# Optimization experiments

Hardware: AMD Instinct MI355X
Metric: run time of the kernel (lower is better)

## Reference

```python
import jax, jax.numpy as jnp
import numpy as np

DIM = 768
NUM_BLOCKS = 4
BLOCK = DIM // NUM_BLOCKS
SCALE = 0.02
LAMBDA = 0.01
EPS = 1e-5


def setup_inputs() -> dict:
    key = jax.random.key(0)
    ks = jax.random.split(key, 6)
    B, H, W = 64, 32, 32
    x = jax.random.normal(ks[0], (B, DIM, H, W), dtype=jnp.float32)
    w1 = jax.random.normal(ks[1], (2, NUM_BLOCKS, BLOCK, BLOCK), dtype=jnp.float32) * SCALE
    w2 = jax.random.normal(ks[2], (2, NUM_BLOCKS, BLOCK, BLOCK), dtype=jnp.float32) * SCALE
    b1 = jax.random.normal(ks[3], (2, NUM_BLOCKS, BLOCK), dtype=jnp.float32) * SCALE
    b2 = jax.random.normal(ks[4], (2, NUM_BLOCKS, BLOCK), dtype=jnp.float32) * SCALE
    gamma = jnp.ones((DIM,), dtype=jnp.float32)
    beta = jnp.zeros((DIM,), dtype=jnp.float32)
    return {"x": x, "w1": w1, "w2": w2, "b1": b1, "b2": b2,
            "gamma": gamma, "beta": beta, "H": H, "W": W}


def _softshrink(s, lam):
    return jnp.where(s > lam, s - lam, jnp.where(s < -lam, s + lam, jnp.zeros_like(s)))


def reference(x, w1, w2, b1, b2, gamma, beta, H, W):
    B, C = x.shape[0], x.shape[1]
    nb, bs = NUM_BLOCKS, C // NUM_BLOCKS
    # (B, C, H, W) -> (B, N, C)
    xt = x.reshape(B, C, H * W).transpose(0, 2, 1)
    residual = xt
    # LayerNorm over channel dim
    mu = jnp.mean(xt, axis=-1, keepdims=True)
    var = jnp.mean(jnp.square(xt - mu), axis=-1, keepdims=True)
    xn = (xt - mu) / jnp.sqrt(var + EPS) * gamma + beta
    # (B, N, nb, bs), FFT2 over (N, nb)
    xf = jnp.fft.fft2(xn.reshape(B, H * W, nb, bs), axes=(1, 2), norm='ortho')
    xr, xi = xf.real, xf.imag

    def mul(u, w):
        return jnp.einsum('bnqd,qdk->bnqk', u, w)  # block-diagonal matmul

    r1 = jax.nn.relu(mul(xr, w1[0]) - mul(xi, w1[1]) + b1[0])
    i1 = jax.nn.relu(mul(xr, w1[1]) + mul(xi, w1[0]) + b1[1])
    r2 = mul(r1, w2[0]) - mul(i1, w2[1]) + b2[0]
    i2 = mul(r1, w2[1]) + mul(i1, w2[0]) + b2[1]
    s = jnp.stack([r2, i2], axis=-1)
    s = _softshrink(s, LAMBDA)
    xc = jax.lax.complex(s[..., 0], s[..., 1])
    y = jnp.fft.ifft2(xc, axes=(1, 2), norm='ortho').real  # cast complex->real keeps real part
    y = y.reshape(B, H * W, C) + residual
    return y.transpose(0, 2, 1).reshape(B, C, H, W)
```

## Files before the change

kernel.cpp:

```cpp
#include <hip/hip_runtime.h>
#include <math.h>

#define BB 64
#define CC 768
#define NN 1024
#define BS 192
#define EPS 1e-5f
#define LAM 0.01f

typedef float  f32x4  __attribute__((ext_vector_type(4)));
typedef short  bf16x8 __attribute__((ext_vector_type(8)));

__device__ inline unsigned f2bf(float x) {
    unsigned u = __float_as_uint(x);
    u += 0x7fff + ((u >> 16) & 1);
    return u >> 16;
}
__device__ inline unsigned pack2(float r, float i) { return f2bf(r) | (f2bf(i) << 16); }
__device__ inline float bflo(unsigned v) { return __uint_as_float(v << 16); }
__device__ inline float bfhi(unsigned v) { return __uint_as_float(v & 0xffff0000u); }

__device__ inline int swz(int i) { return i ^ (((i >> 4) & 3) << 2); }

__global__ __launch_bounds__(512) void ln_stats(const float* __restrict__ x,
                                                float* __restrict__ mu,
                                                float* __restrict__ rstd) {
    int tn = threadIdx.x & 63, tc = threadIdx.x >> 6;
    int n = blockIdx.x * 256 + tn * 4, b = blockIdx.y;
    const float* xp = x + (size_t)b * CC * NN + n;
    f32x4 s = (f32x4)0.f, ss = (f32x4)0.f;
    #pragma unroll 4
    for (int c = tc; c < CC; c += 8) {
        f32x4 v = *(const f32x4*)(xp + (size_t)c * NN);
        s += v; ss += v * v;
    }
    __shared__ f32x4 sm[8][64], sq[8][64];
    sm[tc][tn] = s; sq[tc][tn] = ss;
    __syncthreads();
    if (tc == 0) {
        f32x4 S  = sm[0][tn], SS = sq[0][tn];
        #pragma unroll
        for (int i = 1; i < 8; i++) { S += sm[i][tn]; SS += sq[i][tn]; }
        f32x4 m = S * (1.f / 768.f);
        f32x4 r;
        #pragma unroll
        for (int i = 0; i < 4; i++) {
            float var = SS[i] * (1.f / 768.f) - m[i] * m[i];
            r[i] = rsqrtf(var + EPS);
        }
        *(f32x4*)(mu + (size_t)b * NN + n)   = m;
        *(f32x4*)(rstd + (size_t)b * NN + n) = r;
    }
}

__global__ void fwd_fft(const float* __restrict__ x,
                        const float* __restrict__ mu_, const float* __restrict__ rs_,
                        const float* __restrict__ gamma, const float* __restrict__ beta,
                        unsigned* __restrict__ Xp) {
    __shared__ float2 bufs[4][1024];
    int d = blockIdx.x, b = blockIdx.y, tid = threadIdx.x;

    const float* mp = mu_ + b * NN;
    const float* rp = rs_ + b * NN;
    #pragma unroll
    for (int q = 0; q < 4; q++) {
        int c = q * BS + d;
        float g = gamma[c], be = beta[c];
        const float* xp = x + ((size_t)b * CC + c) * NN;
        #pragma unroll
        for (int k = 0; k < 4; k++) {
            int n = tid + 256 * k;
            float v = (xp[n] - mp[n]) * rp[n] * g + be;
            bufs[q][swz(n)] = make_float2(v, 0.f);
        }
    }
    __syncthreads();

    #pragma unroll
    for (int sL = 0; sL < 4; sL++) {
        const int L = 256 >> (2 * sL);
        int j = tid & (L - 1);
        int base = ((tid - j) << 2) + j;
        float s1, c1;
        __sincosf(-(float)M_PI * 0.5f * (float)j / (float)L, &s1, &c1);
        float c2 = c1 * c1 - s1 * s1, s2 = 2.f * c1 * s1;
        float c3 = c2 * c1 - s2 * s1, s3 = c2 * s1 + s2 * c1;
        #pragma unroll
        for (int q = 0; q < 4; q++) {
            float2 a  = bufs[q][swz(base)];
            float2 bb = bufs[q][swz(base + L)];
            float2 cc = bufs[q][swz(base + 2 * L)];
            float2 dd = bufs[q][swz(base + 3 * L)];
            float t0r = a.x + cc.x, t0i = a.y + cc.y;
            float t1r = a.x - cc.x, t1i = a.y - cc.y;
            float t2r = bb.x + dd.x, t2i = bb.y + dd.y;
            float t3r = bb.x - dd.x, t3i = bb.y - dd.y;
            float X0r = t0r + t2r, X0i = t0i + t2i;
            float X2r = t0r - t2r, X2i = t0i - t2i;
            float X1r = t1r + t3i, X1i = t1i - t3r;
            float X3r = t1r - t3i, X3i = t1i + t3r;
            bufs[q][swz(base)]         = make_float2(X0r, X0i);
            bufs[q][swz(base + L)]     = make_float2(X1r * c1 - X1i * s1, X1r * s1 + X1i * c1);
            bufs[q][swz(base + 2 * L)] = make_float2(X2r * c2 - X2i * s2, X2r * s2 + X2i * c2);
            bufs[q][swz(base + 3 * L)] = make_float2(X3r * c3 - X3i * s3, X3r * s3 + X3i * c3);
        }
        __syncthreads();
    }

    float Xr[4][4], Xi[4][4];
    int i0 = swz(4 * tid);
    #pragma unroll
    for (int q = 0; q < 4; q++) {
        const float4* p = (const float4*)&bufs[q][i0];
        float4 u0 = p[0], u1 = p[1];
        float t0r = u0.x + u1.x, t0i = u0.y + u1.y;
        float t1r = u0.x - u1.x, t1i = u0.y - u1.y;
        float t2r = u0.z + u1.z, t2i = u0.w + u1.w;
        float t3r = u0.z - u1.z, t3i = u0.w - u1.w;
        Xr[q][0] = t0r + t2r; Xi[q][0] = t0i + t2i;
        Xr[q][1] = t1r + t3i; Xi[q][1] = t1i - t3r;
        Xr[q][2] = t0r - t2r; Xi[q][2] = t0i - t2i;
        Xr[q][3] = t1r - t3i; Xi[q][3] = t1i + t3r;
    }
    const float sc = 1.f / 64.f;
    unsigned o0[4], o1[4], o2[4], o3[4];
    #pragma unroll
    for (int m = 0; m < 4; m++) {
        float x0r = Xr[0][m], x0i = Xi[0][m];
        float x1r = Xr[1][m], x1i = Xi[1][m];
        float x2r = Xr[2][m], x2i = Xi[2][m];
        float x3r = Xr[3][m], x3i = Xi[3][m];
        float X0r = x0r + x1r + x2r + x3r, X0i = x0i + x1i + x2i + x3i;
        float X2r = x0r - x1r + x2r - x3r, X2i = x0i - x1i + x2i - x3i;
        float X1r = x0r + x1i - x2r - x3i, X1i = x0i - x1r - x2i + x3r;
        float X3r = x0r - x1i - x2r + x3i, X3i = x0i + x1r - x2i - x3r;
        o0[m] = pack2(X0r * sc, X0i * sc);
        o1[m] = pack2(X1r * sc, X1i * sc);
        o2[m] = pack2(X2r * sc, X2i * sc);
        o3[m] = pack2(X3r * sc, X3i * sc);
    }
    size_t qs = (size_t)BS * NN;
    int cs = ((d >> 2) & 3) << 3;
    size_t base = (((size_t)b * 4) * BS + d) * NN + ((4 * tid) ^ cs);
    *(uint4*)(Xp + base)          = make_uint4(o0[0], o0[1], o0[2], o0[3]);
    *(uint4*)(Xp + base + qs)     = make_uint4(o1[0], o1[1], o1[2], o1[3]);
    *(uint4*)(Xp + base + 2 * qs) = make_uint4(o2[0], o2[1], o2[2], o2[3]);
    *(uint4*)(Xp + base + 3 * qs) = make_uint4(o3[0], o3[1], o3[2], o3[3]);
}

__global__ void pack_b(const float* __restrict__ w, unsigned* __restrict__ Bp) {
    int ch = blockIdx.x, nblk = blockIdx.y, q = blockIdx.z;
    size_t tile = (size_t)((q * 3 + nblk) * 12 + ch);
    const float* wr = w + (size_t)q * BS * BS;
    const float* wi = w + (size_t)(4 + q) * BS * BS;
    for (int r = 0; r < 8; r++) {
        int idx = r * 256 + threadIdx.x;
        int jl = idx & 127, dd = idx >> 7;
        int j = nblk * 128 + jl;
        int h = j >> 1;
        int dg = ch * 16 + dd;
        float Wr = wr[(size_t)dg * BS + h];
        float Wi = wi[(size_t)dg * BS + h];
        unsigned v = (j & 1) ? pack2(Wi, Wr) : pack2(Wr, -Wi);
        int col = ((dd >> 2) ^ ((jl >> 1) & 3)) * 4 + (dd & 3);
        Bp[tile * 2048 + jl * 16 + col] = v;
    }
}

template <int ACT>
__global__ __launch_bounds__(256) void gemm_mlp(const unsigned* __restrict__ Ap,
                                                const unsigned* __restrict__ Bp,
                                                const float* __restrict__ bias,
                                                unsigned* __restrict__ Cp) {
    __shared__ unsigned sa[2][2048];
    __shared__ unsigned sb[2][2048];

    const int mblk = blockIdx.x;
    const int nblk = blockIdx.y;
    const int bq   = blockIdx.z;
    const int q    = bq & 3;
    const int tid  = threadIdx.x;
    const int wave = tid >> 6;
    const int lane = tid & 63;
    const int l15  = lane & 15;
    const int quad = lane >> 4;
    const int wm   = (wave & 1) * 64;
    const int wn   = (wave >> 1) * 64;

    const unsigned* a_base = Ap + ((size_t)bq * BS) * NN + mblk * 128;
    const size_t a_lane = (size_t)(lane >> 5) * NN + (lane & 31) * 4;
    const unsigned* b_tiles = Bp + (size_t)((q * 3 + nblk) * 12) * 2048;
    const int fgrp = (quad ^ ((l15 >> 1) & 3)) * 16;
    const int r0 = wave * 4;

    f32x4 acc[4][4];
    #pragma unroll
    for (int i = 0; i < 4; i++)
        #pragma unroll
        for (int j = 0; j < 4; j++)
            acc[i][j] = (f32x4)0.f;

    auto STAGE = [&](int ch, int buf) {
        const unsigned* ga = a_base + (size_t)(ch * 16) * NN;
        __builtin_amdgcn_global_load_lds(
            (const __attribute__((address_space(1))) unsigned*)(ga + (size_t)r0 * NN + a_lane),
            (__attribute__((address_space(3))) unsigned*)(&sa[buf][r0 * 128]), 16, 0, 0);
        __builtin_amdgcn_global_load_lds(
            (const __attribute__((address_space(1))) unsigned*)(ga + (size_t)(r0 + 2) * NN + a_lane),
            (__attribute__((address_space(3))) unsigned*)(&sa[buf][(r0 + 2) * 128]), 16, 0, 0);
        const unsigned* gb = b_tiles + (size_t)ch * 2048 + wave * 512;
        __builtin_amdgcn_global_load_lds(
            (const __attribute__((address_space(1))) unsigned*)(gb + lane * 4),
            (__attribute__((address_space(3))) unsigned*)(&sb[buf][wave * 512]), 16, 0, 0);
        __builtin_amdgcn_global_load_lds(
            (const __attribute__((address_space(1))) unsigned*)(gb + 256 + lane * 4),
            (__attribute__((address_space(3))) unsigned*)(&sb[buf][wave * 512 + 256]), 16, 0, 0);
    };

    STAGE(0, 0);

    #pragma unroll
    for (int ch = 0; ch < 12; ch++) {
        const int buf = ch & 1;
        __syncthreads();
        if (ch < 11) STAGE(ch + 1, buf ^ 1);

        bf16x8 af[4], bfr[4];
        const unsigned* sap = sa[buf];
        #pragma unroll
        for (int t = 0; t < 4; t++) {
            int cx = (wm + t * 16 + l15) ^ (quad << 3);
            union { unsigned u[4]; bf16x8 v; } au;
            #pragma unroll
            for (int g = 0; g < 4; g++)
                au.u[g] = sap[(quad * 4 + g) * 128 + cx];
            af[t] = au.v;
            bfr[t] = *(const bf16x8*)((const char*)sb[buf] + (wn + t * 16 + l15) * 64 + fgrp);
        }
        #pragma unroll
        for (int tn = 0; tn < 4; tn++)
            #pragma unroll
            for (int tm = 0; tm < 4; tm++)
                acc[tn][tm] = __builtin_amdgcn_mfma_f32_16x16x32_bf16(bfr[tn], af[tm], acc[tn][tm], 0, 0, 0);
    }

    #pragma unroll
    for (int tn = 0; tn < 4; tn++) {
        int jb = wn + tn * 16 + quad * 4;
        int hg = nblk * 64 + (jb >> 1);
        float b0r = bias[q * BS + hg];
        float b0i = bias[768 + q * BS + hg];
        float b1r = bias[q * BS + hg + 1];
        float b1i = bias[768 + q * BS + hg + 1];
        int s0 = ((hg >> 2) & 3) << 3;
        int s1 = (((hg + 1) >> 2) & 3) << 3;
        size_t row0 = ((size_t)bq * BS + hg) * NN + mblk * 128;
        #pragma unroll
        for (int tm = 0; tm < 4; tm++) {
            int mcol = wm + tm * 16 + l15;
            f32x4 a = acc[tn][tm];
            float v0 = a[0] + b0r, v1 = a[1] + b0i;
            float v2 = a[2] + b1r, v3 = a[3] + b1i;
            if (ACT == 0) {
                v0 = fmaxf(v0, 0.f); v1 = fmaxf(v1, 0.f);
                v2 = fmaxf(v2, 0.f); v3 = fmaxf(v3, 0.f);
            } else {
                v0 = (v0 > LAM) ? (v0 - LAM) : ((v0 < -LAM) ? (v0 + LAM) : 0.f);
                v1 = (v1 > LAM) ? (v1 - LAM) : ((v1 < -LAM) ? (v1 + LAM) : 0.f);
                v2 = (v2 > LAM) ? (v2 - LAM) : ((v2 < -LAM) ? (v2 + LAM) : 0.f);
                v3 = (v3 > LAM) ? (v3 - LAM) : ((v3 < -LAM) ? (v3 + LAM) : 0.f);
            }
            Cp[row0 + (mcol ^ s0)]      = pack2(v0, v1);
            Cp[row0 + NN + (mcol ^ s1)] = pack2(v2, v3);
        }
    }
}

__global__ void inv_fft(const float* __restrict__ x,
                        const unsigned* __restrict__ Yp,
                        float* __restrict__ out) {
    __shared__ float2 bufs[4][1024];
    int d = blockIdx.x, b = blockIdx.y, tid = threadIdx.x;

    float Ar[4][4], Ai[4][4];
    size_t qs = (size_t)BS * NN;
    int cs = ((d >> 2) & 3) << 3;
    size_t rowb = (((size_t)b * 4) * BS + d) * NN + ((4 * tid) ^ cs);
    #pragma unroll
    for (int q = 0; q < 4; q++) {
        uint4 v = *(const uint4*)(Yp + rowb + (size_t)q * qs);
        Ar[q][0] = bflo(v.x); Ai[q][0] = bfhi(v.x);
        Ar[q][1] = bflo(v.y); Ai[q][1] = bfhi(v.y);
        Ar[q][2] = bflo(v.z); Ai[q][2] = bfhi(v.z);
        Ar[q][3] = bflo(v.w); Ai[q][3] = bfhi(v.w);
    }
    #pragma unroll
    for (int m = 0; m < 4; m++) {
        float x0r = Ar[0][m], x0i = Ai[0][m];
        float x1r = Ar[1][m], x1i = Ai[1][m];
        float x2r = Ar[2][m], x2i = Ai[2][m];
        float x3r = Ar[3][m], x3i = Ai[3][m];
        float Y0r = x0r + x1r + x2r + x3r, Y0i = x0i + x1i + x2i + x3i;
        float Y2r = x0r - x1r + x2r - x3r, Y2i = x0i - x1i + x2i - x3i;
        float Y1r = x0r - x1i - x2r + x3i, Y1i = x0i + x1r - x2i - x3r;
        float Y3r = x0r + x1i - x2r - x3i, Y3i = x0i - x1r - x2i + x3r;
        Ar[0][m] = Y0r; Ai[0][m] = Y0i;
        Ar[1][m] = Y1r; Ai[1][m] = Y1i;
        Ar[2][m] = Y2r; Ai[2][m] = Y2i;
        Ar[3][m] = Y3r; Ai[3][m] = Y3i;
    }
    int i0 = swz(4 * tid);
    #pragma unroll
    for (int q = 0; q < 4; q++) {
        float t0r = Ar[q][0] + Ar[q][2], t0i = Ai[q][0] + Ai[q][2];
        float t1r = Ar[q][0] - Ar[q][2], t1i = Ai[q][0] - Ai[q][2];
        float t2r = Ar[q][1] + Ar[q][3], t2i = Ai[q][1] + Ai[q][3];
        float t3r = Ar[q][1] - Ar[q][3], t3i = Ai[q][1] - Ai[q][3];
        float4* p = (float4*)&bufs[q][i0];
        p[0] = make_float4(t0r + t2r, t0i + t2i, t1r - t3i, t1i + t3r);
        p[1] = make_float4(t0r - t2r, t0i - t2i, t1r + t3i, t1i - t3r);
    }
    __syncthreads();

    #pragma unroll
    for (int sL = 0; sL < 4; sL++) {
        const int L = 4 << (2 * sL);
        int j = tid & (L - 1);
        int base = ((tid - j) << 2) + j;
        float s1, c1;
        __sincosf((float)M_PI * 0.5f * (float)j / (float)L, &s1, &c1);
        float c2 = c1 * c1 - s1 * s1, s2 = 2.f * c1 * s1;
        float c3 = c2 * c1 - s2 * s1, s3 = c2 * s1 + s2 * c1;
        #pragma unroll
        for (int q = 0; q < 4; q++) {
            float2 y0 = bufs[q][swz(base)];
            float2 y1 = bufs[q][swz(base + L)];
            float2 y2 = bufs[q][swz(base + 2 * L)];
            float2 y3 = bufs[q][swz(base + 3 * L)];
            float A1r = y1.x * c1 - y1.y * s1, A1i = y1.x * s1 + y1.y * c1;
            float A2r = y2.x * c2 - y2.y * s2, A2i = y2.x * s2 + y2.y * c2;
            float A3r = y3.x * c3 - y3.y * s3, A3i = y3.x * s3 + y3.y * c3;
            float t0r = y0.x + A2r, t0i = y0.y + A2i;
            float t1r = y0.x - A2r, t1i = y0.y - A2i;
            float t2r = A1r + A3r, t2i = A1i + A3i;
            float t3r = A1r - A3r, t3i = A1i - A3i;
            bufs[q][swz(base)]         = make_float2(t0r + t2r, t0i + t2i);
            bufs[q][swz(base + L)]     = make_float2(t1r - t3i, t1i + t3r);
            bufs[q][swz(base + 2 * L)] = make_float2(t0r - t2r, t0i - t2i);
            bufs[q][swz(base + 3 * L)] = make_float2(t1r + t3i, t1i - t3r);
        }
        __syncthreads();
    }

    const float sc = 1.f / 64.f;
    #pragma unroll
    for (int q = 0; q < 4; q++) {
        size_t row = (((size_t)b * 4 + q) * BS + d) * NN;
        const float* xp = x + row;
        #pragma unroll
        for (int k = 0; k < 4; k++) {
            int n = tid + 256 * k;
            out[row + n] = bufs[q][swz(n)].x * sc + xp[n];
        }
    }
}

extern "C" void kernel_launch(void* const* d_in, const int* in_sizes, int n_in,
                              void* d_out, int out_size, void* d_ws, size_t ws_size,
                              hipStream_t stream) {
    const float* x     = (const float*)d_in[0];
    const float* w1    = (const float*)d_in[1];
    const float* w2    = (const float*)d_in[2];
    const float* b1    = (const float*)d_in[3];
    const float* b2    = (const float*)d_in[4];
    const float* gamma = (const float*)d_in[5];
    const float* beta  = (const float*)d_in[6];

    unsigned* Xp = (unsigned*)d_ws;
    float* mu    = (float*)d_ws + (size_t)BB * CC * NN;
    float* rstd  = mu + (size_t)BB * NN;
    unsigned* Bp1 = (unsigned*)(rstd + (size_t)BB * NN);
    unsigned* Bp2 = Bp1 + (size_t)4 * 3 * 12 * 2048;
    unsigned* Hp = (unsigned*)d_out;
    unsigned* Yp = Xp;

    pack_b<<<dim3(12, 3, 4), 256, 0, stream>>>(w1, Bp1);
    pack_b<<<dim3(12, 3, 4), 256, 0, stream>>>(w2, Bp2);
    ln_stats<<<dim3(NN / 256, BB), 512, 0, stream>>>(x, mu, rstd);
    fwd_fft<<<dim3(BS, BB), 256, 0, stream>>>(x, mu, rstd, gamma, beta, Xp);
    gemm_mlp<0><<<dim3(8, 3, 256), 256, 0, stream>>>(Xp, Bp1, b1, Hp);
    gemm_mlp<1><<<dim3(8, 3, 256), 256, 0, stream>>>(Hp, Bp2, b2, Yp);
    inv_fft<<<dim3(BS, BB), 256, 0, stream>>>(x, Yp, (float*)d_out);
}
```

Before: 798.6 us.

## Drop LDS staging in GEMM and load MFMA fragments directly from global

Removes the double-buffered LDS staging, the barriers and the XOR swizzles from the block-diagonal GEMM. Each lane now reads its A and B fragments straight from global memory, and the producer/consumer layouts (forward FFT pack, weight pack, epilogue store, inverse FFT read) are unswizzled to match. The aim is to cut barrier and LDS overhead, at the cost of losing shared reuse across waves. A fragments become scattered 4-byte loads with strided rows, and there is no prefetch overlap.

```diff
diff --git a/kernel.cpp b/kernel.cpp
--- a/kernel.cpp
+++ b/kernel.cpp
@@ -140,8 +140,7 @@
         o3[m] = pack2(X3r * sc, X3i * sc);
     }
     size_t qs = (size_t)BS * NN;
-    int cs = ((d >> 2) & 3) << 3;
-    size_t base = (((size_t)b * 4) * BS + d) * NN + ((4 * tid) ^ cs);
+    size_t base = (((size_t)b * 4) * BS + d) * NN + 4 * tid;
     *(uint4*)(Xp + base)          = make_uint4(o0[0], o0[1], o0[2], o0[3]);
     *(uint4*)(Xp + base + qs)     = make_uint4(o1[0], o1[1], o1[2], o1[3]);
     *(uint4*)(Xp + base + 2 * qs) = make_uint4(o2[0], o2[1], o2[2], o2[3]);
@@ -162,8 +161,7 @@
         float Wr = wr[(size_t)dg * BS + h];
         float Wi = wi[(size_t)dg * BS + h];
         unsigned v = (j & 1) ? pack2(Wi, Wr) : pack2(Wr, -Wi);
-        int col = ((dd >> 2) ^ ((jl >> 1) & 3)) * 4 + (dd & 3);
-        Bp[tile * 2048 + jl * 16 + col] = v;
+        Bp[tile * 2048 + jl * 16 + dd] = v;
     }
 }
 
@@ -172,9 +170,6 @@
                                                 const unsigned* __restrict__ Bp,
                                                 const float* __restrict__ bias,
                                                 unsigned* __restrict__ Cp) {
-    __shared__ unsigned sa[2][2048];
-    __shared__ unsigned sb[2][2048];
-
     const int mblk = blockIdx.x;
     const int nblk = blockIdx.y;
     const int bq   = blockIdx.z;
@@ -187,11 +182,8 @@
     const int wm   = (wave & 1) * 64;
     const int wn   = (wave >> 1) * 64;
 
-    const unsigned* a_base = Ap + ((size_t)bq * BS) * NN + mblk * 128;
-    const size_t a_lane = (size_t)(lane >> 5) * NN + (lane & 31) * 4;
-    const unsigned* b_tiles = Bp + (size_t)((q * 3 + nblk) * 12) * 2048;
-    const int fgrp = (quad ^ ((l15 >> 1) & 3)) * 16;
-    const int r0 = wave * 4;
+    const unsigned* a_lane = Ap + ((size_t)bq * BS + quad * 4) * NN + mblk * 128 + wm + l15;
+    const unsigned* b_lane = Bp + (size_t)((q * 3 + nblk) * 12) * 2048 + (wn + l15) * 16 + quad * 4;
 
     f32x4 acc[4][4];
     #pragma unroll
@@ -200,42 +192,21 @@
         for (int j = 0; j < 4; j++)
             acc[i][j] = (f32x4)0.f;
 
-    auto STAGE = [&](int ch, int buf) {
-        const unsigned* ga = a_base + (size_t)(ch * 16) * NN;
-        __builtin_amdgcn_global_load_lds(
-            (const __attribute__((address_space(1))) unsigned*)(ga + (size_t)r0 * NN + a_lane),
-            (__attribute__((address_space(3))) unsigned*)(&sa[buf][r0 * 128]), 16, 0, 0);
-        __builtin_amdgcn_global_load_lds(
-            (const __attribute__((address_space(1))) unsigned*)(ga + (size_t)(r0 + 2) * NN + a_lane),
-            (__attribute__((address_space(3))) unsigned*)(&sa[buf][(r0 + 2) * 128]), 16, 0, 0);
-        const unsigned* gb = b_tiles + (size_t)ch * 2048 + wave * 512;
-        __builtin_amdgcn_global_load_lds(
-            (const __attribute__((address_space(1))) unsigned*)(gb + lane * 4),
-            (__attribute__((address_space(3))) unsigned*)(&sb[buf][wave * 512]), 16, 0, 0);
-        __builtin_amdgcn_global_load_lds(
-            (const __attribute__((address_space(1))) unsigned*)(gb + 256 + lane * 4),
-            (__attribute__((address_space(3))) unsigned*)(&sb[buf][wave * 512 + 256]), 16, 0, 0);
-    };
-
-    STAGE(0, 0);
-
     #pragma unroll
     for (int ch = 0; ch < 12; ch++) {
-        const int buf = ch & 1;
-        __syncthreads();
-        if (ch < 11) STAGE(ch + 1, buf ^ 1);
-
+        const unsigned* ap = a_lane + (size_t)(ch * 16) * NN;
+        const unsigned* bp = b_lane + ch * 2048;
         bf16x8 af[4], bfr[4];
-        const unsigned* sap = sa[buf];
         #pragma unroll
         for (int t = 0; t < 4; t++) {
-            int cx = (wm + t * 16 + l15) ^ (quad << 3);
             union { unsigned u[4]; bf16x8 v; } au;
             #pragma unroll
             for (int g = 0; g < 4; g++)
-                au.u[g] = sap[(quad * 4 + g) * 128 + cx];
+                au.u[g] = ap[(size_t)g * NN + t * 16];
             af[t] = au.v;
-            bfr[t] = *(const bf16x8*)((const char*)sb[buf] + (wn + t * 16 + l15) * 64 + fgrp);
+            union { uint4 u4; bf16x8 v; } bu;
+            bu.u4 = *(const uint4*)(bp + t * 256);
+            bfr[t] = bu.v;
         }
         #pragma unroll
         for (int tn = 0; tn < 4; tn++)
@@ -252,8 +223,6 @@
         float b0i = bias[768 + q * BS + hg];
         float b1r = bias[q * BS + hg + 1];
         float b1i = bias[768 + q * BS + hg + 1];
-        int s0 = ((hg >> 2) & 3) << 3;
-        int s1 = (((hg + 1) >> 2) & 3) << 3;
         size_t row0 = ((size_t)bq * BS + hg) * NN + mblk * 128;
         #pragma unroll
         for (int tm = 0; tm < 4; tm++) {
@@ -270,8 +239,8 @@
                 v2 = (v2 > LAM) ? (v2 - LAM) : ((v2 < -LAM) ? (v2 + LAM) : 0.f);
                 v3 = (v3 > LAM) ? (v3 - LAM) : ((v3 < -LAM) ? (v3 + LAM) : 0.f);
             }
-            Cp[row0 + (mcol ^ s0)]      = pack2(v0, v1);
-            Cp[row0 + NN + (mcol ^ s1)] = pack2(v2, v3);
+            Cp[row0 + mcol]      = pack2(v0, v1);
+            Cp[row0 + NN + mcol] = pack2(v2, v3);
         }
     }
 }
@@ -284,8 +253,7 @@
 
     float Ar[4][4], Ai[4][4];
     size_t qs = (size_t)BS * NN;
-    int cs = ((d >> 2) & 3) << 3;
-    size_t rowb = (((size_t)b * 4) * BS + d) * NN + ((4 * tid) ^ cs);
+    size_t rowb = (((size_t)b * 4) * BS + d) * NN + 4 * tid;
     #pragma unroll
     for (int q = 0; q < 4; q++) {
         uint4 v = *(const uint4*)(Yp + rowb + (size_t)q * qs);
```

Measured after the change: 889.8 us. 1.11x slower.
